# Kernel optimization log

Measured on AMD Instinct MI355X. Metric: run time of the kernel, lower is better.

## Reference

```python
import jax, jax.numpy as jnp
import numpy as np

B, S, HID = 1, 2048, 2048
NH = 16
QL, KVL = 1536, 512
DN, DR, DV = 128, 64, 128
DQ = DN + DR  # 192
IH, ID = 4, 128
TOPK = 1024
EPS = 1e-6
THETA = 10000.0


def rope_interleaved(x, cos, sin):
    # x: (b,s,h,d); cos/sin: (s,d//2); pairs are (x[...,2i], x[...,2i+1])
    xr = x[..., 0::2]
    xi = x[..., 1::2]
    c = cos[None, :, None, :]
    s = sin[None, :, None, :]
    yr = xr * c - xi * s
    yi = xr * s + xi * c
    return jnp.stack([yr, yi], axis=-1).reshape(x.shape)


def rope_noninterleaved(x, cos, sin):
    # rotate-half style: pairs are (x[...,i], x[...,i+d/2])
    d = x.shape[-1] // 2
    x1, x2 = x[..., :d], x[..., d:]
    c = cos[None, :, None, :]
    s = sin[None, :, None, :]
    return jnp.concatenate([x1 * c - x2 * s, x1 * s + x2 * c], axis=-1)


def rmsnorm(x, w):
    var = jnp.mean(x * x, axis=-1, keepdims=True)
    return w * (x * jax.lax.rsqrt(var + EPS))


def layernorm(x, g, b):
    mu = jnp.mean(x, axis=-1, keepdims=True)
    var = jnp.mean((x - mu) ** 2, axis=-1, keepdims=True)
    return (x - mu) * jax.lax.rsqrt(var + EPS) * g + b


def setup_inputs() -> dict:
    key = jax.random.key(0)
    ks = jax.random.split(key, 12)
    std = 0.02
    x = jax.random.normal(ks[0], (B, S, HID), jnp.float32)
    pos = jnp.arange(S, dtype=jnp.float32)
    inv_freq = THETA ** (-jnp.arange(0, DR, 2, dtype=jnp.float32) / DR)
    ang = pos[:, None] * inv_freq[None, :]  # (S, DR//2)
    cos, sin = jnp.cos(ang), jnp.sin(ang)
    mask = jnp.where(jnp.tril(jnp.ones((S, S), bool)), 0.0, -1e9).astype(jnp.float32)
    return {
        "x": x, "cos": cos, "sin": sin, "mask": mask,
        "Wq_a": jax.random.normal(ks[1], (HID, QL), jnp.float32) * std,
        "q_norm_w": jnp.ones((QL,), jnp.float32),
        "Wq_b": jax.random.normal(ks[2], (QL, NH * DQ), jnp.float32) * std,
        "Wkv_a": jax.random.normal(ks[3], (HID, KVL + DR), jnp.float32) * std,
        "kv_norm_w": jnp.ones((KVL,), jnp.float32),
        "Wkv_b": jax.random.normal(ks[4], (KVL, NH * (DN + DV)), jnp.float32) * std,
        "Wo": jax.random.normal(ks[5], (NH * DV, HID), jnp.float32) * std,
        "IWq_b": jax.random.normal(ks[6], (QL, IH * ID), jnp.float32) * std,
        "IWk": jax.random.normal(ks[7], (HID, ID), jnp.float32) * std,
        "Ik_norm_w": jnp.ones((ID,), jnp.float32),
        "Ik_norm_b": jnp.zeros((ID,), jnp.float32),
        "IWproj": jax.random.normal(ks[8], (HID, IH), jnp.float32) * std,
    }


def indexer(x, qr, cos, sin, mask, IWq_b, IWk, Ik_norm_w, Ik_norm_b, IWproj):
    b, s, _ = x.shape
    q = (qr @ IWq_b).reshape(b, s, IH, ID)
    q_pe, q_nope = q[..., :DR], q[..., DR:]
    q_pe = rope_noninterleaved(q_pe, cos, sin)
    q = jnp.concatenate([q_pe, q_nope], axis=-1)
    k = layernorm(x @ IWk, Ik_norm_w, Ik_norm_b)  # (b,s,ID)
    k_pe = rope_noninterleaved(k[:, :, None, :DR], cos, sin)[:, :, 0]
    k = jnp.concatenate([k_pe, k[..., DR:]], axis=-1)
    weights = (x @ IWproj) * (IH ** -0.5) * (ID ** -0.5)  # (b,s,IH)
    logits = jax.nn.relu(jnp.einsum('bthd,bsd->btsh', q, k))
    index_score = jnp.einsum('btsh,bth->bts', logits, weights)
    index_score = index_score + mask[None]
    k_top = min(TOPK, s)
    topk_idx = jax.lax.top_k(index_score, k_top)[1]  # (b,s,k)
    bi = jnp.arange(b)[:, None, None]
    si = jnp.arange(s)[None, :, None]
    index_mask = jnp.full((b, s, s), -1e9, jnp.float32).at[bi, si, topk_idx].set(0.0)
    return index_mask


def reference(x, cos, sin, mask, Wq_a, q_norm_w, Wq_b, Wkv_a, kv_norm_w, Wkv_b, Wo,
              IWq_b, IWk, Ik_norm_w, Ik_norm_b, IWproj):
    b, s, _ = x.shape
    qr = rmsnorm(x @ Wq_a, q_norm_w)  # (b,s,QL)
    q = (qr @ Wq_b).reshape(b, s, NH, DQ)
    q_nope, q_pe = q[..., :DN], q[..., DN:]
    q_pe = rope_interleaved(q_pe, cos, sin)
    q = jnp.concatenate([q_nope, q_pe], axis=-1)
    kv_full = x @ Wkv_a
    kv, k_pe = kv_full[..., :KVL], kv_full[..., KVL:]
    kv = rmsnorm(kv, kv_norm_w)
    k_pe = rope_interleaved(k_pe[:, :, None, :], cos, sin)  # (b,s,1,DR)
    kv_exp = (kv @ Wkv_b).reshape(b, s, NH, DN + DV)
    k_nope, v = kv_exp[..., :DN], kv_exp[..., DN:]
    k = jnp.concatenate([k_nope, jnp.broadcast_to(k_pe, (b, s, NH, DR))], axis=-1)
    scores = jnp.einsum('bshd,bthd->bsht', q, k) * (DQ ** -0.5)
    index_mask = indexer(x, qr, cos, sin, mask, IWq_b, IWk, Ik_norm_w, Ik_norm_b, IWproj)
    scores = scores + index_mask[:, :, None, :] + mask[None, :, None, :]
    probs = jax.nn.softmax(scores, axis=-1)
    out = jnp.einsum('bsht,bthd->bshd', probs, v).reshape(b, s, NH * DV)
    return out @ Wo
```

## Files before the change

kernel.cpp:

```cpp
#include <hip/hip_runtime.h>
#include <math.h>
#include <stdint.h>

#define S 2048
#define HID 2048
#define NH 16
#define QL 1536
#define KVL 512
#define DN 128
#define DR 64
#define DV 128
#define DQ 192
#define IH 4
#define ID 128
#define TOPK 1024

#define N1 2244
#define N2 3584

#define WT_OFF3 ((size_t)N2 * QL)
#define WT_OFF4 (WT_OFF3 + (size_t)4096 * KVL)
#define WT_TOTAL (WT_OFF4 + (size_t)2048 * 2048)

#define CDIV(a,b) (((a)+(b)-1)/(b))

typedef float f32x4 __attribute__((ext_vector_type(4)));
typedef short bf16x8 __attribute__((ext_vector_type(8)));

__device__ __forceinline__ ushort f2b(float f) {
    uint32_t u = __float_as_uint(f);
    u += 0x7fffu + ((u >> 16) & 1u);
    return (ushort)(u >> 16);
}

#define GLL16(g, l)                                                            \
    __builtin_amdgcn_global_load_lds(                                          \
        (const __attribute__((address_space(1))) void*)(g),                    \
        (__attribute__((address_space(3))) void*)(l), 16, 0, 0)

__global__ __launch_bounds__(256) void gemm_bt(const ushort* __restrict__ A,
                                               const ushort* __restrict__ BT,
                                               float* __restrict__ C,
                                               int M, int N, int K) {
    __shared__ ushort As[2][128 * 64];
    __shared__ ushort Bs[2][128 * 64];
    const int tid = threadIdx.x;
    const int w = tid >> 6, l = tid & 63;
    const int quad = l >> 4, lane = l & 15;
    const int row0 = blockIdx.y * 128, col0 = blockIdx.x * 128;
    const int wr = (w >> 1) * 64, wc = (w & 1) * 64;
    f32x4 acc[4][4];
#pragma unroll
    for (int i = 0; i < 4; i++)
#pragma unroll
        for (int j = 0; j < 4; j++) acc[i][j] = (f32x4)0.f;

    const int r32 = tid >> 3;
    const int csw = (((tid & 7) ^ (r32 & 7)) * 8);
    const ushort* pA[4];
    const ushort* pB[4];
#pragma unroll
    for (int p = 0; p < 4; p++) {
        pA[p] = A + (size_t)(row0 + p * 32 + r32) * K + csw;
        int bn = col0 + p * 32 + r32; if (bn > N - 1) bn = N - 1;
        pB[p] = BT + (size_t)bn * K + csw;
    }
    const int doff = r32 * 64 + (tid & 7) * 8;

#define STG64(k0, s)                                                           \
    {                                                                          \
        _Pragma("unroll")                                                      \
        for (int p = 0; p < 4; p++) {                                          \
            GLL16(pA[p] + (k0), &As[s][p * 2048 + doff]);                      \
            GLL16(pB[p] + (k0), &Bs[s][p * 2048 + doff]);                      \
        }                                                                      \
    }

    const int nt = K >> 6;
    STG64(0, 0);
    asm volatile("s_waitcnt vmcnt(0)" ::: "memory");
    __builtin_amdgcn_s_barrier();

    const int xsw = (lane & 7) << 3;
    int cur = 0;
    for (int t = 0; t < nt; ++t) {
        if (t + 1 < nt) STG64((t + 1) * 64, cur ^ 1);
#pragma unroll
        for (int kk = 0; kk < 2; kk++) {
            const int fo = (kk * 32 + quad * 8) ^ xsw;
            bf16x8 af[4], bf[4];
#pragma unroll
            for (int mi = 0; mi < 4; mi++)
                af[mi] = *(const bf16x8*)(&As[cur][(wr + mi * 16 + lane) * 64 + fo]);
#pragma unroll
            for (int ni = 0; ni < 4; ni++)
                bf[ni] = *(const bf16x8*)(&Bs[cur][(wc + ni * 16 + lane) * 64 + fo]);
#pragma unroll
            for (int mi = 0; mi < 4; mi++)
#pragma unroll
                for (int ni = 0; ni < 4; ni++)
                    acc[mi][ni] = __builtin_amdgcn_mfma_f32_16x16x32_bf16(af[mi], bf[ni], acc[mi][ni], 0, 0, 0);
        }
        asm volatile("s_waitcnt vmcnt(0)" ::: "memory");
        __builtin_amdgcn_s_barrier();
        cur ^= 1;
    }
#pragma unroll
    for (int mi = 0; mi < 4; mi++)
#pragma unroll
        for (int ni = 0; ni < 4; ni++)
#pragma unroll
            for (int r = 0; r < 4; r++) {
                int row = row0 + wr + mi * 16 + quad * 4 + r;
                int col = col0 + wc + ni * 16 + lane;
                if (col < N) C[(size_t)row * N + col] = acc[mi][ni][r];
            }
}

__global__ __launch_bounds__(256) void gemm_bt_h(const ushort* __restrict__ A,
                                                 const ushort* __restrict__ BT,
                                                 ushort* __restrict__ C,
                                                 int M, int N, int K) {
    __shared__ ushort As[2][128 * 64];
    __shared__ ushort Bs[2][128 * 64];
    const int tid = threadIdx.x;
    const int w = tid >> 6, l = tid & 63;
    const int quad = l >> 4, lane = l & 15;
    const int row0 = blockIdx.y * 128, col0 = blockIdx.x * 128;
    const int wr = (w >> 1) * 64, wc = (w & 1) * 64;
    f32x4 acc[4][4];
#pragma unroll
    for (int i = 0; i < 4; i++)
#pragma unroll
        for (int j = 0; j < 4; j++) acc[i][j] = (f32x4)0.f;

    const int r32 = tid >> 3;
    const int csw = (((tid & 7) ^ (r32 & 7)) * 8);
    const ushort* pA[4];
    const ushort* pB[4];
#pragma unroll
    for (int p = 0; p < 4; p++) {
        pA[p] = A + (size_t)(row0 + p * 32 + r32) * K + csw;
        int bn = col0 + p * 32 + r32; if (bn > N - 1) bn = N - 1;
        pB[p] = BT + (size_t)bn * K + csw;
    }
    const int doff = r32 * 64 + (tid & 7) * 8;

    const int nt = K >> 6;
    STG64(0, 0);
    asm volatile("s_waitcnt vmcnt(0)" ::: "memory");
    __builtin_amdgcn_s_barrier();

    const int xsw = (lane & 7) << 3;
    int cur = 0;
    for (int t = 0; t < nt; ++t) {
        if (t + 1 < nt) STG64((t + 1) * 64, cur ^ 1);
#pragma unroll
        for (int kk = 0; kk < 2; kk++) {
            const int fo = (kk * 32 + quad * 8) ^ xsw;
            bf16x8 af[4], bf[4];
#pragma unroll
            for (int mi = 0; mi < 4; mi++)
                af[mi] = *(const bf16x8*)(&As[cur][(wr + mi * 16 + lane) * 64 + fo]);
#pragma unroll
            for (int ni = 0; ni < 4; ni++)
                bf[ni] = *(const bf16x8*)(&Bs[cur][(wc + ni * 16 + lane) * 64 + fo]);
#pragma unroll
            for (int mi = 0; mi < 4; mi++)
#pragma unroll
                for (int ni = 0; ni < 4; ni++)
                    acc[mi][ni] = __builtin_amdgcn_mfma_f32_16x16x32_bf16(af[mi], bf[ni], acc[mi][ni], 0, 0, 0);
        }
        asm volatile("s_waitcnt vmcnt(0)" ::: "memory");
        __builtin_amdgcn_s_barrier();
        cur ^= 1;
    }
#pragma unroll
    for (int mi = 0; mi < 4; mi++)
#pragma unroll
        for (int ni = 0; ni < 4; ni++)
#pragma unroll
            for (int r = 0; r < 4; r++) {
                int row = row0 + wr + mi * 16 + quad * 4 + r;
                int col = col0 + wc + ni * 16 + lane;
                if (col < N) C[(size_t)row * N + col] = f2b(acc[mi][ni][r]);
            }
}

__device__ __forceinline__ void wtrans_body(const float* W, ushort* WT, int K, int N,
                                            int k0, int n0) {
    __shared__ float t[64][65];
    int rr = threadIdx.x >> 6, cc = threadIdx.x & 63;
#pragma unroll
    for (int p = 0; p < 16; p++) {
        int k = k0 + p * 4 + rr, n = n0 + cc;
        t[p * 4 + rr][cc] = (k < K && n < N) ? W[(size_t)k * N + n] : 0.f;
    }
    __syncthreads();
#pragma unroll
    for (int p = 0; p < 16; p++) {
        int n = n0 + p * 4 + rr, k = k0 + cc;
        if (n < N && k < K) WT[(size_t)n * K + k] = f2b(t[cc][p * 4 + rr]);
    }
}

__global__ __launch_bounds__(256) void prep1(const float* __restrict__ x,
                                             ushort* __restrict__ xb,
                                             const float* __restrict__ W0,
                                             const float* __restrict__ W1,
                                             const float* __restrict__ W2,
                                             const float* __restrict__ W3,
                                             ushort* __restrict__ WT) {
    const int id = blockIdx.x;
    if (id < 1152) {
        const float* W; int N; size_t off; int loc;
        if (id < 768)       { W = W0; N = 1536; off = 0;                  loc = id; }
        else if (id < 1056) { W = W1; N = 576;  off = (size_t)1536 * HID; loc = id - 768; }
        else if (id < 1120) { W = W2; N = 128;  off = (size_t)2112 * HID; loc = id - 1056; }
        else                { W = W3; N = 4;    off = (size_t)2240 * HID; loc = id - 1120; }
        wtrans_body(W, WT + off, HID, N, (loc & 31) * 64, (loc >> 5) * 64);
    } else {
        const int i = (id - 1152) * 256 + threadIdx.x;
        float4 v = *(const float4*)(x + (size_t)i * 4);
        uint32_t lo = (uint32_t)f2b(v.x) | ((uint32_t)f2b(v.y) << 16);
        uint32_t hi = (uint32_t)f2b(v.z) | ((uint32_t)f2b(v.w) << 16);
        *(uint2*)(xb + (size_t)i * 4) = make_uint2(lo, hi);
    }
}

__global__ __launch_bounds__(256) void prep2(const float* __restrict__ W0,
                                             const float* __restrict__ W1,
                                             const float* __restrict__ Wkvb,
                                             const float* __restrict__ Wo,
                                             ushort* __restrict__ WT) {
    const int id = blockIdx.x;
    const float* W; int K, N, nx; size_t off; int loc;
    if (id < 1152)      { W = W0;   K = QL;   N = 3072; nx = 24; off = 0;                 loc = id; }
    else if (id < 1344) { W = W1;   K = QL;   N = 512;  nx = 24; off = (size_t)3072 * QL; loc = id - 1152; }
    else if (id < 1856) { W = Wkvb; K = KVL;  N = 4096; nx = 8;  off = WT_OFF3;           loc = id - 1344; }
    else                { W = Wo;   K = 2048; N = 2048; nx = 32; off = WT_OFF4;           loc = id - 1856; }
    wtrans_body(W, WT + off, K, N, (loc % nx) * 64, (loc / nx) * 64);
}

__global__ __launch_bounds__(256) void post_c1(const float* __restrict__ C1,
                                               const float* __restrict__ qw,
                                               const float* __restrict__ kvw,
                                               const float* __restrict__ ikg,
                                               const float* __restrict__ ikb,
                                               const float* __restrict__ cosb,
                                               const float* __restrict__ sinb,
                                               ushort* __restrict__ qrb,
                                               ushort* __restrict__ kvnb,
                                               float* __restrict__ kpe,
                                               float* __restrict__ kiT) {
    const int t = blockIdx.x, tid = threadIdx.x;
    const float* row = C1 + (size_t)t * N1;
    __shared__ float red[256];
    __shared__ float kis[128];
    float ss = 0.f;
    for (int i = tid; i < 1536; i += 256) { float v = row[i]; ss += v * v; }
    red[tid] = ss; __syncthreads();
    for (int st = 128; st > 0; st >>= 1) { if (tid < st) red[tid] += red[tid + st]; __syncthreads(); }
    float sq = rsqrtf(red[0] / 1536.f + 1e-6f);
    __syncthreads();
    float s2 = 0.f;
    for (int i = tid; i < 512; i += 256) { float v = row[1536 + i]; s2 += v * v; }
    red[tid] = s2; __syncthreads();
    for (int st = 128; st > 0; st >>= 1) { if (tid < st) red[tid] += red[tid + st]; __syncthreads(); }
    float skv = rsqrtf(red[0] / 512.f + 1e-6f);
    __syncthreads();
    float kv_ = (tid < 128) ? row[2112 + tid] : 0.f;
    red[tid] = kv_; __syncthreads();
    for (int st = 128; st > 0; st >>= 1) { if (tid < st) red[tid] += red[tid + st]; __syncthreads(); }
    float mu = red[0] / 128.f;
    __syncthreads();
    red[tid] = kv_ * kv_; __syncthreads();
    for (int st = 128; st > 0; st >>= 1) { if (tid < st) red[tid] += red[tid + st]; __syncthreads(); }
    float var = red[0] / 128.f - mu * mu;
    for (int i = tid; i < 1536; i += 256) qrb[(size_t)t * QL + i] = f2b(row[i] * sq * qw[i]);
    for (int i = tid; i < 512; i += 256)  kvnb[(size_t)t * KVL + i] = f2b(row[1536 + i] * skv * kvw[i]);
    if (tid < 32) {
        float c = cosb[t * 32 + tid], s = sinb[t * 32 + tid];
        float xr = row[2048 + 2 * tid], xi = row[2048 + 2 * tid + 1];
        kpe[t * 64 + 2 * tid]     = xr * c - xi * s;
        kpe[t * 64 + 2 * tid + 1] = xr * s + xi * c;
    }
    if (tid < 128) kis[tid] = (kv_ - mu) * rsqrtf(var + 1e-6f) * ikg[tid] + ikb[tid];
    __syncthreads();
    if (tid < 128) {
        float outv;
        if (tid < 32) {
            float c = cosb[t * 32 + tid], s = sinb[t * 32 + tid];
            outv = kis[tid] * c - kis[tid + 32] * s;
        } else if (tid < 64) {
            int j = tid - 32;
            float c = cosb[t * 32 + j], s = sinb[t * 32 + j];
            outv = kis[j] * s + kis[tid] * c;
        } else {
            outv = kis[tid];
        }
        kiT[(size_t)tid * S + t] = outv;
    }
}

__global__ __launch_bounds__(256) void post_c2(float* __restrict__ C2,
                                               const float* __restrict__ cosb,
                                               const float* __restrict__ sinb,
                                               ushort* __restrict__ qb) {
    const int t = blockIdx.x, tid = threadIdx.x;
    __shared__ float cs[32], sn[32];
    if (tid < 32) { cs[tid] = cosb[t * 32 + tid]; sn[tid] = sinb[t * 32 + tid]; }
    __syncthreads();
    const float sc = 0.10412775370051047f;
    const float* src0 = C2 + (size_t)t * N2;
    for (int i = tid; i < NH * 96; i += 256) {
        int h = i / 96, p = i % 96;
        const float* src = src0 + h * 192;
        ushort* dst = qb + ((size_t)h * S + t) * 192;
        if (p < 64) {
            dst[2 * p]     = f2b(src[2 * p] * sc);
            dst[2 * p + 1] = f2b(src[2 * p + 1] * sc);
        } else {
            int j = p - 64;
            float c = cs[j], s = sn[j];
            float xr = src[128 + 2 * j], xi = src[128 + 2 * j + 1];
            dst[128 + 2 * j]     = f2b((xr * c - xi * s) * sc);
            dst[128 + 2 * j + 1] = f2b((xr * s + xi * c) * sc);
        }
    }
    if (tid < 128) {
        int h = tid >> 5, j = tid & 31;
        float* p = C2 + (size_t)t * N2 + 3072 + h * 128;
        float c = cs[j], s = sn[j];
        float x1 = p[j], x2 = p[j + 32];
        p[j] = x1 * c - x2 * s;
        p[j + 32] = x1 * s + x2 * c;
    }
}

__global__ __launch_bounds__(256) void pack_kv(const ushort* __restrict__ kvexp_h,
                                               const float* __restrict__ kpe,
                                               ushort* __restrict__ kb,
                                               ushort* __restrict__ vT) {
    __shared__ ushort t[64][136];
    const int s0 = blockIdx.x * 64, h = blockIdx.y, tid = threadIdx.x;
    const int row = tid >> 2, c = tid & 3;
    const ushort* src = kvexp_h + (size_t)(s0 + row) * 4096 + h * 256;
    ushort* kbr = kb + ((size_t)h * S + s0 + row) * 192;
#pragma unroll
    for (int i = 0; i < 4; i++) {
        int off = c * 32 + i * 8;
        *(uint4*)(kbr + off) = *(const uint4*)(src + off);
        *(uint4*)(&t[row][off]) = *(const uint4*)(src + 128 + off);
    }
    const float* kp = kpe + (size_t)(s0 + row) * 64 + c * 16;
#pragma unroll
    for (int i = 0; i < 16; i++) kbr[128 + c * 16 + i] = f2b(kp[i]);
    __syncthreads();
    const int d = tid >> 1, sh = (tid & 1) * 32;
    ushort* dst = vT + ((size_t)h * 128 + d) * S + s0 + sh;
#pragma unroll
    for (int i = 0; i < 32; i++) dst[i] = t[sh + i][d];
}

__global__ __launch_bounds__(256) void iscore4x4(const float* __restrict__ qi,
                                                 const float* __restrict__ kiT,
                                                 const float* __restrict__ iw,
                                                 float* __restrict__ iscore) {
    const int t0 = blockIdx.x * 4;
    const int s0 = blockIdx.y * 1024;
    if (s0 > t0 + 3) return;
    const int s = s0 + threadIdx.x * 4;
    __shared__ float qsT[4 * ID * 4];
    __shared__ float ws[16];
    for (int i = threadIdx.x; i < 4 * ID * 4; i += 256) {
        int tt = i & 3, hd = i >> 2;
        qsT[hd * 4 + tt] = qi[(size_t)(t0 + tt) * N2 + hd];
    }
    if (threadIdx.x < 16) {
        int tt = threadIdx.x >> 2, h = threadIdx.x & 3;
        ws[threadIdx.x] = iw[(size_t)(t0 + tt) * N1 + h] * 0.04419417382415922f;
    }
    __syncthreads();
    if (s > t0 + 3) return;
    float a[4][4][4];
#pragma unroll
    for (int tt = 0; tt < 4; tt++)
#pragma unroll
        for (int h = 0; h < 4; h++)
#pragma unroll
            for (int c = 0; c < 4; c++) a[tt][h][c] = 0.f;
    for (int d = 0; d < ID; d++) {
        float4 kv = *(const float4*)(kiT + (size_t)d * S + s);
#pragma unroll
        for (int h = 0; h < 4; h++) {
            float4 qv = *(const float4*)(&qsT[(h * ID + d) * 4]);
            a[0][h][0] += qv.x * kv.x; a[0][h][1] += qv.x * kv.y;
            a[0][h][2] += qv.x * kv.z; a[0][h][3] += qv.x * kv.w;
            a[1][h][0] += qv.y * kv.x; a[1][h][1] += qv.y * kv.y;
            a[1][h][2] += qv.y * kv.z; a[1][h][3] += qv.y * kv.w;
            a[2][h][0] += qv.z * kv.x; a[2][h][1] += qv.z * kv.y;
            a[2][h][2] += qv.z * kv.z; a[2][h][3] += qv.z * kv.w;
            a[3][h][0] += qv.w * kv.x; a[3][h][1] += qv.w * kv.y;
            a[3][h][2] += qv.w * kv.z; a[3][h][3] += qv.w * kv.w;
        }
    }
#pragma unroll
    for (int tt = 0; tt < 4; tt++) {
        const int t = t0 + tt;
        if (s > t) continue;
#pragma unroll
        for (int c = 0; c < 4; c++) {
            if (s + c > t) break;
            float sc = fmaxf(a[tt][0][c], 0.f) * ws[tt * 4 + 0] +
                       fmaxf(a[tt][1][c], 0.f) * ws[tt * 4 + 1] +
                       fmaxf(a[tt][2][c], 0.f) * ws[tt * 4 + 2] +
                       fmaxf(a[tt][3][c], 0.f) * ws[tt * 4 + 3];
            iscore[(size_t)t * S + s + c] = sc;
        }
    }
}

__device__ inline unsigned sortable_u32(float f) {
    unsigned u = __float_as_uint(f);
    return (u & 0x80000000u) ? ~u : (u | 0x80000000u);
}

__global__ __launch_bounds__(256) void topk_mask(const float* __restrict__ iscore,
                                                 uint32_t* __restrict__ msk) {
    int t = blockIdx.x, tid = threadIdx.x;
    uint32_t* mrow = msk + (size_t)t * 64;
    if (t < TOPK) {
        if (tid < 64) {
            int full = (t + 1) >> 5;
            uint32_t wv2 = (tid < full) ? 0xFFFFFFFFu : 0u;
            if (tid == full) { int rem = (t + 1) & 31; wv2 = rem ? ((1u << rem) - 1u) : 0u; }
            mrow[tid] = wv2;
        }
        return;
    }
    const float* row = iscore + (size_t)t * S;
    const int n = t + 1;
    const int wv = tid >> 6, lane = tid & 63;
    __shared__ int hist[4][256];
    __shared__ int wtot[4];
    __shared__ int bsel, ksel;
    __shared__ uint32_t bytes[256];

    int jb = tid * 8;
    float4 v0 = *(const float4*)(row + jb);
    float4 v1 = *(const float4*)(row + jb + 4);
    uint32_t lsu[8];
    {
        float vvv[8] = {v0.x, v0.y, v0.z, v0.w, v1.x, v1.y, v1.z, v1.w};
#pragma unroll
        for (int i = 0; i < 8; i++)
            lsu[i] = (jb + i < n) ? sortable_u32(vvv[i]) : 0u;
    }
    unsigned prefix = 0, prefmask = 0;
    int k = TOPK;
    for (int pass = 0; pass < 4; pass++) {
        int shift = 24 - pass * 8;
#pragma unroll
        for (int r = 0; r < 4; r++) hist[r][tid] = 0;
        __syncthreads();
#pragma unroll
        for (int i = 0; i < 8; i++) {
            uint32_t u = lsu[i];
            if ((u & prefmask) == prefix) atomicAdd(&hist[wv][(u >> shift) & 255], 1);
        }
        __syncthreads();
        int h = hist[0][tid] + hist[1][tid] + hist[2][tid] + hist[3][tid];
        int x = h;
#pragma unroll
        for (int off = 1; off < 64; off <<= 1) {
            int tmp = __shfl_down(x, off, 64);
            if (lane + off < 64) x += tmp;
        }
        if (lane == 0) wtot[wv] = x;
        __syncthreads();
        int add = 0;
#pragma unroll
        for (int w2 = 1; w2 < 4; w2++) if (w2 > wv) add += wtot[w2];
        x += add;
        int snext = x - h;
        if (x >= k && snext < k) { bsel = tid; ksel = k - snext; }
        __syncthreads();
        prefix |= ((unsigned)bsel) << shift;
        prefmask |= 0xFFu << shift;
        k = ksel;
        __syncthreads();
    }
    const unsigned u_thr = prefix;
    const int need = k;
    uint32_t gtbits = 0, eqbits = 0;
    int eqcnt = 0;
#pragma unroll
    for (int i = 0; i < 8; i++) {
        uint32_t u = lsu[i];
        if (u > u_thr) gtbits |= 1u << i;
        else if (u == u_thr) { eqbits |= 1u << i; eqcnt++; }
    }
    {
        int x = eqcnt;
#pragma unroll
        for (int off = 1; off < 64; off <<= 1) {
            int tmp = __shfl_up(x, off, 64);
            if (lane >= off) x += tmp;
        }
        if (lane == 63) wtot[wv] = x;
        __syncthreads();
        int add = 0;
#pragma unroll
        for (int w2 = 0; w2 < 3; w2++) if (w2 < wv) add += wtot[w2];
        x += add;
        int room = need - (x - eqcnt);
        uint32_t keep = 0;
#pragma unroll
        for (int i = 0; i < 8; i++)
            if ((eqbits >> i) & 1u) { if (room > 0) { keep |= 1u << i; room--; } }
        bytes[tid] = gtbits | keep;
    }
    __syncthreads();
    if (tid < 64)
        mrow[tid] = bytes[tid * 4] | (bytes[tid * 4 + 1] << 8) |
                    (bytes[tid * 4 + 2] << 16) | (bytes[tid * 4 + 3] << 24);
}

__global__ __launch_bounds__(256, 2) void fattn10(const ushort* __restrict__ qb,
                                                  const ushort* __restrict__ kb,
                                                  const ushort* __restrict__ vT,
                                                  const uint32_t* __restrict__ msk,
                                                  float* __restrict__ Opart,
                                                  float* __restrict__ mlbuf) {
    __shared__ ushort Ks[24 * 512];
    __shared__ ushort Vs[16 * 512];
    __shared__ ushort Pm[4][16 * 72];
    const int tid = threadIdx.x;
    const int w = tid >> 6, l = tid & 63, quad = l >> 4, lane = l & 15;
    const int b = blockIdx.x;
    const int r8 = b & 7, j = b >> 3;
    const int h = r8 + 8 * (j & 1);
    const int idx = j >> 1;
    const int pair = idx & 15, part = idx >> 4;
    const int ta = pair, tb = 31 - pair, nA = ta + 1;
    const int vlo = part * 11, vhi = vlo + 11;
    const int qa0 = ta * 64, qb0 = tb * 64;

    bf16x8 qfa[6], qfb[6];
    {
        const ushort* qpa = qb + ((size_t)h * S + qa0 + w * 16 + lane) * 192;
        const ushort* qpb = qb + ((size_t)h * S + qb0 + w * 16 + lane) * 192;
#pragma unroll
        for (int ks = 0; ks < 6; ks++) {
            qfa[ks] = *(const bf16x8*)(qpa + ks * 32 + quad * 8);
            qfb[ks] = *(const bf16x8*)(qpb + ks * 32 + quad * 8);
        }
    }
    f32x4 oa[8], ob[8];
#pragma unroll
    for (int i = 0; i < 8; i++) { oa[i] = (f32x4)0.f; ob[i] = (f32x4)0.f; }
    float la[4], lb[4];
#pragma unroll
    for (int r = 0; r < 4; r++) { la[r] = 0.f; lb[r] = 0.f; }

    ushort* pw = &Pm[w][0];
    const ushort* kbase = kb + (size_t)h * S * 192;
    const ushort* vbase = vT + (size_t)h * 128 * S;

    for (int kt = 0; kt <= tb; kt++) {
        const int idxB = (kt <= ta) ? 2 * kt : kt + nA;
        const int hasA = (kt <= ta);
        const int idxA = 2 * kt + 1;
        const bool doB = (idxB >= vlo && idxB < vhi);
        const bool doA = hasA && (idxA >= vlo && idxA < vhi);
        if (!(doA || doB)) continue;
        const int s0 = kt * 64;
        __syncthreads();
#pragma unroll
        for (int ii = 0; ii < 6; ii++) {
            const int i = w * 6 + ii;
            const int ks = i >> 2, kq = i & 3;
            const ushort* src = kbase + (size_t)(s0 + kq * 16 + lane) * 192 + ks * 32 + quad * 8;
            GLL16(src, Ks + i * 512 + l * 8);
        }
#pragma unroll
        for (int ii = 0; ii < 4; ii++) {
            const int i = w * 4 + ii;
            const int k2 = i >> 3, nt = i & 7;
            const ushort* src = vbase + (size_t)(nt * 16 + lane) * S + s0 + k2 * 32 + quad * 8;
            GLL16(src, Vs + i * 512 + l * 8);
        }
        __syncthreads();

#pragma unroll
        for (int pass = 0; pass < 2; pass++) {
            if (pass == 0 && !doA) continue;
            if (pass == 1 && !doB) continue;
            const bf16x8* qf = (pass == 0) ? qfa : qfb;
            f32x4* oacc      = (pass == 0) ? oa : ob;
            float* ll        = (pass == 0) ? la : lb;
            const int q0t    = (pass == 0) ? qa0 : qb0;

            f32x4 sc[4];
#pragma unroll
            for (int kq = 0; kq < 4; kq++) {
                sc[kq] = (f32x4)0.f;
#pragma unroll
                for (int ks = 0; ks < 6; ks++) {
                    bf16x8 bfr = *(const bf16x8*)(Ks + (ks * 4 + kq) * 512 + quad * 128 + lane * 8);
                    sc[kq] = __builtin_amdgcn_mfma_f32_16x16x32_bf16(qf[ks], bfr, sc[kq], 0, 0, 0);
                }
            }
            uint32_t w0[4], w1[4];
            {
                const int rowbase = q0t + w * 16 + quad * 4;
#pragma unroll
                for (int r = 0; r < 4; r++) {
                    const uint32_t* mp = msk + (size_t)(rowbase + r) * 64 + (s0 >> 5);
                    w0[r] = mp[0]; w1[r] = mp[1];
                }
            }
#pragma unroll
            for (int kq = 0; kq < 4; kq++) {
                const int sh = (kq & 1) * 16 + lane;
#pragma unroll
                for (int r = 0; r < 4; r++) {
                    uint32_t word = (kq < 2) ? w0[r] : w1[r];
                    float v = ((word >> sh) & 1u) ? sc[kq][r] : -1e30f;
                    float e = exp2f(v);
                    ll[r] += e;
                    pw[(quad * 4 + r) * 72 + kq * 16 + lane] = f2b(e);
                }
            }

            bf16x8 pfr[2];
#pragma unroll
            for (int k2 = 0; k2 < 2; k2++)
                pfr[k2] = *(const bf16x8*)(pw + lane * 72 + k2 * 32 + quad * 8);
#pragma unroll
            for (int nt = 0; nt < 8; nt++) {
#pragma unroll
                for (int k2 = 0; k2 < 2; k2++) {
                    bf16x8 vfr = *(const bf16x8*)(Vs + ((k2 * 8 + nt) * 4 + quad) * 128 + lane * 8);
                    oacc[nt] = __builtin_amdgcn_mfma_f32_16x16x32_bf16(pfr[k2], vfr, oacc[nt], 0, 0, 0);
                }
            }
        }
    }
#pragma unroll
    for (int off = 1; off < 16; off <<= 1)
#pragma unroll
        for (int r = 0; r < 4; r++) {
            la[r] += __shfl_xor(la[r], off, 64);
            lb[r] += __shfl_xor(lb[r], off, 64);
        }
#pragma unroll
    for (int pass = 0; pass < 2; pass++) {
        const f32x4* oacc = (pass == 0) ? oa : ob;
        const float* ll   = (pass == 0) ? la : lb;
        const int qt      = (pass == 0) ? ta : tb;
        float* Op = Opart + (size_t)((qt * 16 + h) * 3 + part) * (64 * 128);
        float* mlp = mlbuf + (size_t)((qt * 16 + h) * 3 + part) * 128;
#pragma unroll
        for (int nt = 0; nt < 8; nt++)
#pragma unroll
            for (int r = 0; r < 4; r++)
                Op[(w * 16 + quad * 4 + r) * 128 + nt * 16 + lane] = oacc[nt][r];
        if (lane == 0) {
#pragma unroll
            for (int r = 0; r < 4; r++) {
                mlp[(w * 16 + quad * 4 + r) * 2 + 0] = 0.f;
                mlp[(w * 16 + quad * 4 + r) * 2 + 1] = ll[r];
            }
        }
    }
}

__global__ __launch_bounds__(256) void attn_combine(const float* __restrict__ Opart,
                                                    const float* __restrict__ mlbuf,
                                                    ushort* __restrict__ attn_b) {
    const int qt = blockIdx.x, h = blockIdx.y, tid = threadIdx.x;
    const size_t base = ((size_t)qt * 16 + h) * 3;
    const float* Op0 = Opart + base * 8192;
    const float* Op1 = Op0 + 8192;
    const float* Op2 = Op1 + 8192;
    const float* ml0 = mlbuf + base * 128;
    const float* ml1 = ml0 + 128;
    const float* ml2 = ml1 + 128;
#pragma unroll
    for (int i = 0; i < 32; i++) {
        int id = tid + i * 256;
        int row = id >> 7, d = id & 127;
        float m0 = ml0[row * 2], l0 = ml0[row * 2 + 1];
        float m1 = ml1[row * 2], l1 = ml1[row * 2 + 1];
        float m2 = ml2[row * 2], l2 = ml2[row * 2 + 1];
        float m = fmaxf(fmaxf(m0, m1), m2);
        float e0 = exp2f(m0 - m), e1 = exp2f(m1 - m), e2 = exp2f(m2 - m);
        float linv = 1.f / (l0 * e0 + l1 * e1 + l2 * e2);
        float v = (Op0[id] * e0 + Op1[id] * e1 + Op2[id] * e2) * linv;
        attn_b[(size_t)(qt * 64 + row) * 2048 + h * 128 + d] = f2b(v);
    }
}

extern "C" void kernel_launch(void* const* d_in, const int* in_sizes, int n_in,
                              void* d_out, int out_size, void* d_ws, size_t ws_size,
                              hipStream_t stream) {
    const float* x        = (const float*)d_in[0];
    const float* cosb     = (const float*)d_in[1];
    const float* sinb     = (const float*)d_in[2];
    const float* Wq_a     = (const float*)d_in[4];
    const float* q_norm_w = (const float*)d_in[5];
    const float* Wq_b     = (const float*)d_in[6];
    const float* Wkv_a    = (const float*)d_in[7];
    const float* kv_norm_w= (const float*)d_in[8];
    const float* Wkv_b    = (const float*)d_in[9];
    const float* Wo       = (const float*)d_in[10];
    const float* IWq_b    = (const float*)d_in[11];
    const float* IWk      = (const float*)d_in[12];
    const float* Ik_norm_w= (const float*)d_in[13];
    const float* Ik_norm_b= (const float*)d_in[14];
    const float* IWproj   = (const float*)d_in[15];
    float* out = (float*)d_out;

    char* ws = (char*)d_ws;
    size_t o = 0;
    auto take = [&](size_t b) { char* p = ws + o; o += (b + 255) & ~(size_t)255; return p; };
    ushort* xb     = (ushort*)take((size_t)S * HID * 2);
    ushort* qrb    = (ushort*)take((size_t)S * QL * 2);
    ushort* qb     = (ushort*)take((size_t)NH * S * DQ * 2);
    ushort* kvnb   = (ushort*)take((size_t)S * KVL * 2);
    float*  kpe    = (float*)take((size_t)S * DR * 4);
    ushort* kb     = (ushort*)take((size_t)NH * S * DQ * 2);
    ushort* vT     = (ushort*)take((size_t)NH * DV * S * 2);
    uint32_t* msk  = (uint32_t*)take((size_t)S * 64 * 4);
    float*  mlbuf  = (float*)take((size_t)32 * 16 * 3 * 64 * 2 * 4);
    ushort* WTp    = (ushort*)take(WT_TOTAL * 2);
    float*  C1     = (float*)take((size_t)S * N1 * 4);
    char*   big    = take((size_t)32 * 16 * 3 * 8192 * 4 + 1024);
    ushort* kvexp_h= (ushort*)take((size_t)S * 4096 * 2);
    float*  kiT    = (float*)take((size_t)128 * S * 4);
    char*   poolb  = take((size_t)16777216);

    float* C2     = (float*)big;
    float* Opart  = (float*)big;
    float* iscore = (float*)poolb;
    ushort* attn_b = (ushort*)poolb;

    prep1<<<5248, 256, 0, stream>>>(x, xb, Wq_a, Wkv_a, IWk, IWproj, WTp);
    gemm_bt<<<dim3(CDIV(N1, 128), S / 128), 256, 0, stream>>>(xb, WTp, C1, S, N1, HID);
    post_c1<<<S, 256, 0, stream>>>(C1, q_norm_w, kv_norm_w, Ik_norm_w, Ik_norm_b,
                                   cosb, sinb, qrb, kvnb, kpe, kiT);

    prep2<<<2880, 256, 0, stream>>>(Wq_b, IWq_b, Wkv_b, Wo, WTp);
    gemm_bt<<<dim3(N2 / 128, S / 128), 256, 0, stream>>>(qrb, WTp, C2, S, N2, QL);
    post_c2<<<S, 256, 0, stream>>>(C2, cosb, sinb, qb);

    gemm_bt_h<<<dim3(32, S / 128), 256, 0, stream>>>(kvnb, WTp + WT_OFF3, kvexp_h, S, NH * (DN + DV), KVL);
    pack_kv<<<dim3(S / 64, NH), 256, 0, stream>>>(kvexp_h, kpe, kb, vT);

    iscore4x4<<<dim3(S / 4, S / 1024), 256, 0, stream>>>(C2 + 3072, kiT, C1 + 2240, iscore);
    topk_mask<<<S, 256, 0, stream>>>(iscore, msk);

    fattn10<<<768, 256, 0, stream>>>(qb, kb, vT, msk, Opart, mlbuf);
    attn_combine<<<dim3(32, 16), 256, 0, stream>>>(Opart, mlbuf, attn_b);

    gemm_bt<<<dim3(HID / 128, S / 128), 256, 0, stream>>>(attn_b, WTp + WT_OFF4, out, S, HID, NH * DV);

    (void)in_sizes; (void)n_in; (void)out_size; (void)ws_size; (void)o;
}
```

Baseline: 467.3 us.

## Merge independent GEMM, weight-transpose and pack kernels into fewer launches

Moves the C1 weight transposes to a separate region so the first GEMM can run in the same launch as the transposes of the later weights. Merges the Wq_b and Wkv_b GEMMs into one launch, and the post_c2 and pack_kv kernels into another. The aim is to cut kernel launches and let independent work fill the GPU together instead of running back to back. In exchange the merged kernels use larger LDS per block, which may lower occupancy for the transpose blocks, and they need a larger weight buffer.

Result: slower. 484.0 us (+3.6%).

```diff
diff --git a/kernel.cpp b/kernel.cpp
--- a/kernel.cpp
+++ b/kernel.cpp
@@ -20,7 +20,8 @@
 
 #define WT_OFF3 ((size_t)N2 * QL)
 #define WT_OFF4 (WT_OFF3 + (size_t)4096 * KVL)
-#define WT_TOTAL (WT_OFF4 + (size_t)2048 * 2048)
+#define WT_OFF5 (WT_OFF4 + (size_t)2048 * 2048)
+#define WT_TOTAL (WT_OFF5 + (size_t)N1 * HID)
 
 #define CDIV(a,b) (((a)+(b)-1)/(b))
 
@@ -38,16 +39,24 @@
         (const __attribute__((address_space(1))) void*)(g),                    \
         (__attribute__((address_space(3))) void*)(l), 16, 0, 0)
 
-__global__ __launch_bounds__(256) void gemm_bt(const ushort* __restrict__ A,
-                                               const ushort* __restrict__ BT,
-                                               float* __restrict__ C,
-                                               int M, int N, int K) {
-    __shared__ ushort As[2][128 * 64];
-    __shared__ ushort Bs[2][128 * 64];
+#define STG64T(k0, s)                                                          \
+    {                                                                          \
+        _Pragma("unroll")                                                      \
+        for (int p = 0; p < 4; p++) {                                          \
+            GLL16(pA[p] + (k0), As + (s) * 8192 + p * 2048 + doff);            \
+            GLL16(pB[p] + (k0), Bs + (s) * 8192 + p * 2048 + doff);            \
+        }                                                                      \
+    }
+
+template<int HALF>
+__device__ __forceinline__ void gemm_tile(const ushort* __restrict__ A,
+                                          const ushort* __restrict__ BT,
+                                          void* __restrict__ Cv,
+                                          int N, int K, int row0, int col0,
+                                          ushort* As, ushort* Bs) {
     const int tid = threadIdx.x;
     const int w = tid >> 6, l = tid & 63;
     const int quad = l >> 4, lane = l & 15;
-    const int row0 = blockIdx.y * 128, col0 = blockIdx.x * 128;
     const int wr = (w >> 1) * 64, wc = (w & 1) * 64;
     f32x4 acc[4][4];
 #pragma unroll
@@ -67,34 +76,25 @@
     }
     const int doff = r32 * 64 + (tid & 7) * 8;
 
-#define STG64(k0, s)                                                           \
-    {                                                                          \
-        _Pragma("unroll")                                                      \
-        for (int p = 0; p < 4; p++) {                                          \
-            GLL16(pA[p] + (k0), &As[s][p * 2048 + doff]);                      \
-            GLL16(pB[p] + (k0), &Bs[s][p * 2048 + doff]);                      \
-        }                                                                      \
-    }
-
     const int nt = K >> 6;
-    STG64(0, 0);
+    STG64T(0, 0);
     asm volatile("s_waitcnt vmcnt(0)" ::: "memory");
     __builtin_amdgcn_s_barrier();
 
     const int xsw = (lane & 7) << 3;
     int cur = 0;
     for (int t = 0; t < nt; ++t) {
-        if (t + 1 < nt) STG64((t + 1) * 64, cur ^ 1);
+        if (t + 1 < nt) STG64T((t + 1) * 64, cur ^ 1);
 #pragma unroll
         for (int kk = 0; kk < 2; kk++) {
             const int fo = (kk * 32 + quad * 8) ^ xsw;
             bf16x8 af[4], bf[4];
 #pragma unroll
             for (int mi = 0; mi < 4; mi++)
-                af[mi] = *(const bf16x8*)(&As[cur][(wr + mi * 16 + lane) * 64 + fo]);
+                af[mi] = *(const bf16x8*)(As + cur * 8192 + (wr + mi * 16 + lane) * 64 + fo);
 #pragma unroll
             for (int ni = 0; ni < 4; ni++)
-                bf[ni] = *(const bf16x8*)(&Bs[cur][(wc + ni * 16 + lane) * 64 + fo]);
+                bf[ni] = *(const bf16x8*)(Bs + cur * 8192 + (wc + ni * 16 + lane) * 64 + fo);
 #pragma unroll
             for (int mi = 0; mi < 4; mi++)
 #pragma unroll
@@ -113,94 +113,26 @@
             for (int r = 0; r < 4; r++) {
                 int row = row0 + wr + mi * 16 + quad * 4 + r;
                 int col = col0 + wc + ni * 16 + lane;
-                if (col < N) C[(size_t)row * N + col] = acc[mi][ni][r];
+                if (col < N) {
+                    if (HALF) ((ushort*)Cv)[(size_t)row * N + col] = f2b(acc[mi][ni][r]);
+                    else      ((float*)Cv)[(size_t)row * N + col] = acc[mi][ni][r];
+                }
             }
 }
 
-__global__ __launch_bounds__(256) void gemm_bt_h(const ushort* __restrict__ A,
-                                                 const ushort* __restrict__ BT,
-                                                 ushort* __restrict__ C,
-                                                 int M, int N, int K) {
-    __shared__ ushort As[2][128 * 64];
-    __shared__ ushort Bs[2][128 * 64];
-    const int tid = threadIdx.x;
-    const int w = tid >> 6, l = tid & 63;
-    const int quad = l >> 4, lane = l & 15;
-    const int row0 = blockIdx.y * 128, col0 = blockIdx.x * 128;
-    const int wr = (w >> 1) * 64, wc = (w & 1) * 64;
-    f32x4 acc[4][4];
-#pragma unroll
-    for (int i = 0; i < 4; i++)
-#pragma unroll
-        for (int j = 0; j < 4; j++) acc[i][j] = (f32x4)0.f;
-
-    const int r32 = tid >> 3;
-    const int csw = (((tid & 7) ^ (r32 & 7)) * 8);
-    const ushort* pA[4];
-    const ushort* pB[4];
-#pragma unroll
-    for (int p = 0; p < 4; p++) {
-        pA[p] = A + (size_t)(row0 + p * 32 + r32) * K + csw;
-        int bn = col0 + p * 32 + r32; if (bn > N - 1) bn = N - 1;
-        pB[p] = BT + (size_t)bn * K + csw;
-    }
-    const int doff = r32 * 64 + (tid & 7) * 8;
-
-    const int nt = K >> 6;
-    STG64(0, 0);
-    asm volatile("s_waitcnt vmcnt(0)" ::: "memory");
-    __builtin_amdgcn_s_barrier();
-
-    const int xsw = (lane & 7) << 3;
-    int cur = 0;
-    for (int t = 0; t < nt; ++t) {
-        if (t + 1 < nt) STG64((t + 1) * 64, cur ^ 1);
-#pragma unroll
-        for (int kk = 0; kk < 2; kk++) {
-            const int fo = (kk * 32 + quad * 8) ^ xsw;
-            bf16x8 af[4], bf[4];
-#pragma unroll
-            for (int mi = 0; mi < 4; mi++)
-                af[mi] = *(const bf16x8*)(&As[cur][(wr + mi * 16 + lane) * 64 + fo]);
-#pragma unroll
-            for (int ni = 0; ni < 4; ni++)
-                bf[ni] = *(const bf16x8*)(&Bs[cur][(wc + ni * 16 + lane) * 64 + fo]);
-#pragma unroll
-            for (int mi = 0; mi < 4; mi++)
-#pragma unroll
-                for (int ni = 0; ni < 4; ni++)
-                    acc[mi][ni] = __builtin_amdgcn_mfma_f32_16x16x32_bf16(af[mi], bf[ni], acc[mi][ni], 0, 0, 0);
-        }
-        asm volatile("s_waitcnt vmcnt(0)" ::: "memory");
-        __builtin_amdgcn_s_barrier();
-        cur ^= 1;
-    }
-#pragma unroll
-    for (int mi = 0; mi < 4; mi++)
-#pragma unroll
-        for (int ni = 0; ni < 4; ni++)
-#pragma unroll
-            for (int r = 0; r < 4; r++) {
-                int row = row0 + wr + mi * 16 + quad * 4 + r;
-                int col = col0 + wc + ni * 16 + lane;
-                if (col < N) C[(size_t)row * N + col] = f2b(acc[mi][ni][r]);
-            }
-}
-
-__device__ __forceinline__ void wtrans_body(const float* W, ushort* WT, int K, int N,
-                                            int k0, int n0) {
-    __shared__ float t[64][65];
+__device__ __forceinline__ void wtrans_lds(const float* W, ushort* WT, int K, int N,
+                                           int k0, int n0, float* t) {
     int rr = threadIdx.x >> 6, cc = threadIdx.x & 63;
 #pragma unroll
     for (int p = 0; p < 16; p++) {
         int k = k0 + p * 4 + rr, n = n0 + cc;
-        t[p * 4 + rr][cc] = (k < K && n < N) ? W[(size_t)k * N + n] : 0.f;
+        t[(p * 4 + rr) * 65 + cc] = (k < K && n < N) ? W[(size_t)k * N + n] : 0.f;
     }
     __syncthreads();
 #pragma unroll
     for (int p = 0; p < 16; p++) {
         int n = n0 + p * 4 + rr, k = k0 + cc;
-        if (n < N && k < K) WT[(size_t)n * K + k] = f2b(t[cc][p * 4 + rr]);
+        if (n < N && k < K) WT[(size_t)n * K + k] = f2b(t[cc * 65 + p * 4 + rr]);
     }
 }
 
@@ -210,7 +142,8 @@
                                              const float* __restrict__ W1,
                                              const float* __restrict__ W2,
                                              const float* __restrict__ W3,
-                                             ushort* __restrict__ WT) {
+                                             ushort* __restrict__ WTc1) {
+    __shared__ float tb[64 * 65];
     const int id = blockIdx.x;
     if (id < 1152) {
         const float* W; int N; size_t off; int loc;
@@ -218,7 +151,7 @@
         else if (id < 1056) { W = W1; N = 576;  off = (size_t)1536 * HID; loc = id - 768; }
         else if (id < 1120) { W = W2; N = 128;  off = (size_t)2112 * HID; loc = id - 1056; }
         else                { W = W3; N = 4;    off = (size_t)2240 * HID; loc = id - 1120; }
-        wtrans_body(W, WT + off, HID, N, (loc & 31) * 64, (loc >> 5) * 64);
+        wtrans_lds(W, WTc1 + off, HID, N, (loc & 31) * 64, (loc >> 5) * 64, tb);
     } else {
         const int i = (id - 1152) * 256 + threadIdx.x;
         float4 v = *(const float4*)(x + (size_t)i * 4);
@@ -228,18 +161,56 @@
     }
 }
 
-__global__ __launch_bounds__(256) void prep2(const float* __restrict__ W0,
-                                             const float* __restrict__ W1,
-                                             const float* __restrict__ Wkvb,
-                                             const float* __restrict__ Wo,
-                                             ushort* __restrict__ WT) {
+__global__ __launch_bounds__(256) void megaC1(const ushort* __restrict__ xb,
+                                              ushort* __restrict__ WT,
+                                              float* __restrict__ C1,
+                                              const float* __restrict__ Wq_b,
+                                              const float* __restrict__ IWq_b,
+                                              const float* __restrict__ Wkvb,
+                                              const float* __restrict__ Wo) {
+    __shared__ ushort As[2][8192];
+    __shared__ ushort Bs[2][8192];
     const int id = blockIdx.x;
-    const float* W; int K, N, nx; size_t off; int loc;
-    if (id < 1152)      { W = W0;   K = QL;   N = 3072; nx = 24; off = 0;                 loc = id; }
-    else if (id < 1344) { W = W1;   K = QL;   N = 512;  nx = 24; off = (size_t)3072 * QL; loc = id - 1152; }
-    else if (id < 1856) { W = Wkvb; K = KVL;  N = 4096; nx = 8;  off = WT_OFF3;           loc = id - 1344; }
-    else                { W = Wo;   K = 2048; N = 2048; nx = 32; off = WT_OFF4;           loc = id - 1856; }
-    wtrans_body(W, WT + off, K, N, (loc % nx) * 64, (loc / nx) * 64);
+    if (id < 288) {
+        gemm_tile<0>(xb, WT + WT_OFF5, C1, N1, HID, (id / 18) * 128, (id % 18) * 128,
+                     &As[0][0], &Bs[0][0]);
+    } else {
+        const int pid = id - 288;
+        const float* W; int K, N, nx; size_t off; int loc;
+        if (pid < 1152)      { W = Wq_b;  K = QL;   N = 3072; nx = 24; off = 0;                 loc = pid; }
+        else if (pid < 1344) { W = IWq_b; K = QL;   N = 512;  nx = 24; off = (size_t)3072 * QL; loc = pid - 1152; }
+        else if (pid < 1856) { W = Wkvb;  K = KVL;  N = 4096; nx = 8;  off = WT_OFF3;           loc = pid - 1344; }
+        else                 { W = Wo;    K = 2048; N = 2048; nx = 32; off = WT_OFF4;           loc = pid - 1856; }
+        wtrans_lds(W, WT + off, K, N, (loc % nx) * 64, (loc / nx) * 64, (float*)&As[0][0]);
+    }
+}
+
+__global__ __launch_bounds__(256) void megaC2(const ushort* __restrict__ qrb,
+                                              const ushort* __restrict__ kvnb,
+                                              const ushort* __restrict__ WT,
+                                              float* __restrict__ C2,
+                                              ushort* __restrict__ kvexp_h) {
+    __shared__ ushort As[2][8192];
+    __shared__ ushort Bs[2][8192];
+    const int id = blockIdx.x;
+    if (id < 448) {
+        gemm_tile<0>(qrb, WT, C2, N2, QL, (id / 28) * 128, (id % 28) * 128,
+                     &As[0][0], &Bs[0][0]);
+    } else {
+        const int loc = id - 448;
+        gemm_tile<1>(kvnb, WT + WT_OFF3, kvexp_h, 4096, KVL,
+                     (loc / 32) * 128, (loc % 32) * 128, &As[0][0], &Bs[0][0]);
+    }
+}
+
+__global__ __launch_bounds__(256) void gemm_f32(const ushort* __restrict__ A,
+                                                const ushort* __restrict__ BT,
+                                                float* __restrict__ C,
+                                                int N, int K) {
+    __shared__ ushort As[2][8192];
+    __shared__ ushort Bs[2][8192];
+    gemm_tile<0>(A, BT, C, N, K, blockIdx.y * 128, blockIdx.x * 128,
+                 &As[0][0], &Bs[0][0]);
 }
 
 __global__ __launch_bounds__(256) void post_c1(const float* __restrict__ C1,
@@ -303,64 +274,67 @@
     }
 }
 
-__global__ __launch_bounds__(256) void post_c2(float* __restrict__ C2,
-                                               const float* __restrict__ cosb,
-                                               const float* __restrict__ sinb,
-                                               ushort* __restrict__ qb) {
-    const int t = blockIdx.x, tid = threadIdx.x;
+__global__ __launch_bounds__(256) void megaPost(float* __restrict__ C2,
+                                                const float* __restrict__ cosb,
+                                                const float* __restrict__ sinb,
+                                                ushort* __restrict__ qb,
+                                                const ushort* __restrict__ kvexp_h,
+                                                const float* __restrict__ kpe,
+                                                ushort* __restrict__ kb,
+                                                ushort* __restrict__ vT) {
     __shared__ float cs[32], sn[32];
-    if (tid < 32) { cs[tid] = cosb[t * 32 + tid]; sn[tid] = sinb[t * 32 + tid]; }
-    __syncthreads();
-    const float sc = 0.10412775370051047f;
-    const float* src0 = C2 + (size_t)t * N2;
-    for (int i = tid; i < NH * 96; i += 256) {
-        int h = i / 96, p = i % 96;
-        const float* src = src0 + h * 192;
-        ushort* dst = qb + ((size_t)h * S + t) * 192;
-        if (p < 64) {
-            dst[2 * p]     = f2b(src[2 * p] * sc);
-            dst[2 * p + 1] = f2b(src[2 * p + 1] * sc);
-        } else {
-            int j = p - 64;
+    __shared__ ushort tt[64][136];
+    const int id = blockIdx.x, tid = threadIdx.x;
+    if (id < 2048) {
+        const int t = id;
+        if (tid < 32) { cs[tid] = cosb[t * 32 + tid]; sn[tid] = sinb[t * 32 + tid]; }
+        __syncthreads();
+        const float sc = 0.10412775370051047f;
+        const float* src0 = C2 + (size_t)t * N2;
+        for (int i = tid; i < NH * 96; i += 256) {
+            int h = i / 96, p = i % 96;
+            const float* src = src0 + h * 192;
+            ushort* dst = qb + ((size_t)h * S + t) * 192;
+            if (p < 64) {
+                dst[2 * p]     = f2b(src[2 * p] * sc);
+                dst[2 * p + 1] = f2b(src[2 * p + 1] * sc);
+            } else {
+                int j = p - 64;
+                float c = cs[j], s = sn[j];
+                float xr = src[128 + 2 * j], xi = src[128 + 2 * j + 1];
+                dst[128 + 2 * j]     = f2b((xr * c - xi * s) * sc);
+                dst[128 + 2 * j + 1] = f2b((xr * s + xi * c) * sc);
+            }
+        }
+        if (tid < 128) {
+            int h = tid >> 5, j = tid & 31;
+            float* p = C2 + (size_t)t * N2 + 3072 + h * 128;
             float c = cs[j], s = sn[j];
-            float xr = src[128 + 2 * j], xi = src[128 + 2 * j + 1];
-            dst[128 + 2 * j]     = f2b((xr * c - xi * s) * sc);
-            dst[128 + 2 * j + 1] = f2b((xr * s + xi * c) * sc);
-        }
-    }
-    if (tid < 128) {
-        int h = tid >> 5, j = tid & 31;
-        float* p = C2 + (size_t)t * N2 + 3072 + h * 128;
-        float c = cs[j], s = sn[j];
-        float x1 = p[j], x2 = p[j + 32];
-        p[j] = x1 * c - x2 * s;
-        p[j + 32] = x1 * s + x2 * c;
-    }
-}
-
-__global__ __launch_bounds__(256) void pack_kv(const ushort* __restrict__ kvexp_h,
-                                               const float* __restrict__ kpe,
-                                               ushort* __restrict__ kb,
-                                               ushort* __restrict__ vT) {
-    __shared__ ushort t[64][136];
-    const int s0 = blockIdx.x * 64, h = blockIdx.y, tid = threadIdx.x;
-    const int row = tid >> 2, c = tid & 3;
-    const ushort* src = kvexp_h + (size_t)(s0 + row) * 4096 + h * 256;
-    ushort* kbr = kb + ((size_t)h * S + s0 + row) * 192;
-#pragma unroll
-    for (int i = 0; i < 4; i++) {
-        int off = c * 32 + i * 8;
-        *(uint4*)(kbr + off) = *(const uint4*)(src + off);
-        *(uint4*)(&t[row][off]) = *(const uint4*)(src + 128 + off);
-    }
-    const float* kp = kpe + (size_t)(s0 + row) * 64 + c * 16;
-#pragma unroll
-    for (int i = 0; i < 16; i++) kbr[128 + c * 16 + i] = f2b(kp[i]);
-    __syncthreads();
-    const int d = tid >> 1, sh = (tid & 1) * 32;
-    ushort* dst = vT + ((size_t)h * 128 + d) * S + s0 + sh;
-#pragma unroll
-    for (int i = 0; i < 32; i++) dst[i] = t[sh + i][d];
+            float x1 = p[j], x2 = p[j + 32];
+            p[j] = x1 * c - x2 * s;
+            p[j + 32] = x1 * s + x2 * c;
+        }
+    } else {
+        const int loc = id - 2048;
+        const int s0 = (loc & 31) * 64, h = loc >> 5;
+        const int row = tid >> 2, c = tid & 3;
+        const ushort* src = kvexp_h + (size_t)(s0 + row) * 4096 + h * 256;
+        ushort* kbr = kb + ((size_t)h * S + s0 + row) * 192;
+#pragma unroll
+        for (int i = 0; i < 4; i++) {
+            int off = c * 32 + i * 8;
+            *(uint4*)(kbr + off) = *(const uint4*)(src + off);
+            *(uint4*)(&tt[row][off]) = *(const uint4*)(src + 128 + off);
+        }
+        const float* kp = kpe + (size_t)(s0 + row) * 64 + c * 16;
+#pragma unroll
+        for (int i = 0; i < 16; i++) kbr[128 + c * 16 + i] = f2b(kp[i]);
+        __syncthreads();
+        const int d = tid >> 1, sh = (tid & 1) * 32;
+        ushort* dst = vT + ((size_t)h * 128 + d) * S + s0 + sh;
+#pragma unroll
+        for (int i = 0; i < 32; i++) dst[i] = tt[sh + i][d];
+    }
 }
 
 __global__ __launch_bounds__(256) void iscore4x4(const float* __restrict__ qi,
@@ -747,17 +721,15 @@
     float* iscore = (float*)poolb;
     ushort* attn_b = (ushort*)poolb;
 
-    prep1<<<5248, 256, 0, stream>>>(x, xb, Wq_a, Wkv_a, IWk, IWproj, WTp);
-    gemm_bt<<<dim3(CDIV(N1, 128), S / 128), 256, 0, stream>>>(xb, WTp, C1, S, N1, HID);
+    prep1<<<5248, 256, 0, stream>>>(x, xb, Wq_a, Wkv_a, IWk, IWproj, WTp + WT_OFF5);
+
+    megaC1<<<3168, 256, 0, stream>>>(xb, WTp, C1, Wq_b, IWq_b, Wkv_b, Wo);
     post_c1<<<S, 256, 0, stream>>>(C1, q_norm_w, kv_norm_w, Ik_norm_w, Ik_norm_b,
                                    cosb, sinb, qrb, kvnb, kpe, kiT);
 
-    prep2<<<2880, 256, 0, stream>>>(Wq_b, IWq_b, Wkv_b, Wo, WTp);
-    gemm_bt<<<dim3(N2 / 128, S / 128), 256, 0, stream>>>(qrb, WTp, C2, S, N2, QL);
-    post_c2<<<S, 256, 0, stream>>>(C2, cosb, sinb, qb);
-
-    gemm_bt_h<<<dim3(32, S / 128), 256, 0, stream>>>(kvnb, WTp + WT_OFF3, kvexp_h, S, NH * (DN + DV), KVL);
-    pack_kv<<<dim3(S / 64, NH), 256, 0, stream>>>(kvexp_h, kpe, kb, vT);
+    megaC2<<<960, 256, 0, stream>>>(qrb, kvnb, WTp, C2, kvexp_h);
+
+    megaPost<<<2560, 256, 0, stream>>>(C2, cosb, sinb, qb, kvexp_h, kpe, kb, vT);
 
     iscore4x4<<<dim3(S / 4, S / 1024), 256, 0, stream>>>(C2 + 3072, kiT, C1 + 2240, iscore);
     topk_mask<<<S, 256, 0, stream>>>(iscore, msk);
@@ -765,7 +737,7 @@
     fattn10<<<768, 256, 0, stream>>>(qb, kb, vT, msk, Opart, mlbuf);
     attn_combine<<<dim3(32, 16), 256, 0, stream>>>(Opart, mlbuf, attn_b);
 
-    gemm_bt<<<dim3(HID / 128, S / 128), 256, 0, stream>>>(attn_b, WTp + WT_OFF4, out, S, HID, NH * DV);
+    gemm_f32<<<dim3(HID / 128, S / 128), 256, 0, stream>>>(attn_b, WTp + WT_OFF4, out, HID, NH * DV);
 
     (void)in_sizes; (void)n_in; (void)out_size; (void)ws_size; (void)o;
 }
```
